# Kernel optimization log

Hardware: AMD Instinct MI355X
Metric: run time of the kernel (lower is better)

## Reference

```python
import jax, jax.numpy as jnp
import numpy as np

LEVELS = 3

def _db4_filters():
    s3 = np.sqrt(3.0)
    h0 = np.array([(1 + s3), (3 + s3), (3 - s3), (1 - s3)], dtype=np.float32) / (4 * np.sqrt(2.0))
    h1 = np.array([(-1) ** k * h0[3 - k] for k in range(4)], dtype=np.float32)
    return jnp.asarray(h0), jnp.asarray(h1)


def _dwt_1d(x, h0, h1):
    """Single-level db4 DWT along last axis, periodization boundary.
    x: (..., L) with L even -> (lo, hi) each (..., L//2).
    Matches torch: circular pad (left=1, right=2), conv1d (cross-correlation), stride-2 downsample.
    """
    L = x.shape[-1]
    xp = jnp.concatenate([x[..., -1:], x, x[..., :2]], axis=-1)  # circular pad -> (..., L+3)
    # full conv output has length L; only 4 taps, fuse as shifted adds
    lo = h0[0] * xp[..., 0:L] + h0[1] * xp[..., 1:L + 1] + h0[2] * xp[..., 2:L + 2] + h0[3] * xp[..., 3:L + 3]
    hi = h1[0] * xp[..., 0:L] + h1[1] * xp[..., 1:L + 1] + h1[2] * xp[..., 2:L + 2] + h1[3] * xp[..., 3:L + 3]
    return lo[..., ::2], hi[..., ::2]


def _dwt_2d(x, h0, h1):
    """x: (B,C,H,W) -> LL,LH,HL,HH each (B,C,H//2,W//2). Separable: rows (W) then cols (H)."""
    Lr, Hr = _dwt_1d(x, h0, h1)                       # (B,C,H,W/2)
    Lr_t = jnp.swapaxes(Lr, -1, -2)                   # (B,C,W/2,H)
    Hr_t = jnp.swapaxes(Hr, -1, -2)
    LL, LH = _dwt_1d(Lr_t, h0, h1)                    # (B,C,W/2,H/2)
    HL, HH = _dwt_1d(Hr_t, h0, h1)
    LL = jnp.swapaxes(LL, -1, -2)                     # (B,C,H/2,W/2)
    LH = jnp.swapaxes(LH, -1, -2)
    HL = jnp.swapaxes(HL, -1, -2)
    HH = jnp.swapaxes(HH, -1, -2)
    return LL, LH, HL, HH


def _forward(x):
    h0, h1 = _db4_filters()
    details = []  # (LH, HL, HH) per level, level 0 = finest
    cur = x
    for _ in range(LEVELS):
        LL, LH, HL, HH = _dwt_2d(cur, h0, h1)
        details.append((LH, HL, HH))
        cur = LL
    # coeffs_to_im: tile LL top-left, then wrap detail subbands coarsest->finest
    out = cur
    for level in reversed(range(LEVELS)):
        LH, HL, HH = details[level]
        top = jnp.concatenate([out, LH], axis=-1)
        bot = jnp.concatenate([HL, HH], axis=-1)
        out = jnp.concatenate([top, bot], axis=-2)
    return out


def setup_inputs() -> dict:
    key = jax.random.key(0)
    x = jax.random.normal(key, (8, 16, 512, 512), dtype=jnp.float32)
    return {"x": x}


def reference(x):
    return _forward(x)
```

## Files before the change

### kernel.cpp

```cpp
#include <hip/hip_runtime.h>


constexpr int TI = 16;
constexpr int TJ = 32;
constexpr int ROWS = 2 * TI + 2;
constexpr int COLS = 2 * TJ + 2;
constexpr int LDS_STRIDE = COLS + 2;

__global__ __launch_bounds__(256)
void dwt_level(const float* __restrict__ src, int N,
               float* __restrict__ out,
               float* __restrict__ ll, int ll_rs, size_t ll_cs)
{
    const int S = N >> 1;
    const int mask = N - 1;
    __shared__ float tile[ROWS][LDS_STRIDE];

    const int tx = threadIdx.x;
    const int ty = threadIdx.y;
    const int tid = ty * 32 + tx;
    const int j0 = blockIdx.x * TJ;
    const int i0 = blockIdx.y * TI;
    const int ch = blockIdx.z;

    const float* s = src + (size_t)ch * N * N;
    const int gr0 = 2 * i0 - 1;
    const int gc0 = 2 * j0 - 1;

    for (int k = tid; k < ROWS * COLS; k += 256) {
        const int r = k / COLS;
        const int c = k - r * COLS;
        const int gr = (gr0 + r) & mask;
        const int gc = (gc0 + c) & mask;
        tile[r][c] = s[(size_t)gr * N + gc];
    }
    __syncthreads();

    const float h0[4] = { 0.4829629131445341f,  0.8365163037378079f,
                          0.2241438680420134f, -0.1294095225512604f };
    const float h1[4] = { -0.1294095225512604f, -0.2241438680420134f,
                           0.8365163037378079f, -0.4829629131445341f };

    float* outc = out + (size_t)ch * (512 * 512);
    float* llc  = ll  + (size_t)ch * ll_cs;

    #pragma unroll
    for (int rr = 0; rr < 2; ++rr) {
        const int i = ty + rr * 8;
        const int j = tx;
        float a_ll = 0.f, a_lh = 0.f, a_hl = 0.f, a_hh = 0.f;
        #pragma unroll
        for (int p = 0; p < 4; ++p) {
            const float v0 = tile[2 * i + p][2 * j + 0];
            const float v1 = tile[2 * i + p][2 * j + 1];
            const float v2 = tile[2 * i + p][2 * j + 2];
            const float v3 = tile[2 * i + p][2 * j + 3];
            const float lo = h0[0] * v0 + h0[1] * v1 + h0[2] * v2 + h0[3] * v3;
            const float hi = h1[0] * v0 + h1[1] * v1 + h1[2] * v2 + h1[3] * v3;
            a_ll += h0[p] * lo;
            a_lh += h1[p] * lo;
            a_hl += h0[p] * hi;
            a_hh += h1[p] * hi;
        }
        const int gi = i0 + i;
        const int gj = j0 + j;
        llc[(size_t)gi * ll_rs + gj]            = a_ll;
        outc[(size_t)gi * 512 + (S + gj)]       = a_lh;
        outc[(size_t)(S + gi) * 512 + gj]       = a_hl;
        outc[(size_t)(S + gi) * 512 + (S + gj)] = a_hh;
    }
}

extern "C" void kernel_launch(void* const* d_in, const int* in_sizes, int n_in,
                              void* d_out, int out_size, void* d_ws, size_t ws_size,
                              hipStream_t stream) {
    const float* x = (const float*)d_in[0];
    float* out = (float*)d_out;
    const int C = in_sizes[0] / (512 * 512);

    float* ll1 = (float*)d_ws;
    float* ll2 = ll1 + (size_t)C * 256 * 256;

    dim3 blk(32, 8);
    dwt_level<<<dim3(256 / TJ, 256 / TI, C), blk, 0, stream>>>(
        x, 512, out, ll1, 256, (size_t)256 * 256);
    dwt_level<<<dim3(128 / TJ, 128 / TI, C), blk, 0, stream>>>(
        ll1, 256, out, ll2, 128, (size_t)128 * 128);
    dwt_level<<<dim3(64 / TJ, 64 / TI, C), blk, 0, stream>>>(
        ll2, 128, out, out, 512, (size_t)512 * 512);
}
```

Before: 265.8 us.

## Fuse all three DWT levels into one kernel with LDS-resident intermediates

Replaces three per-level kernel launches with a single kernel. Each block loads a 64x128 input tile plus halo (using float4 loads) into LDS, computes the level-1 LL subband into a second LDS buffer, then level-2 LL into a third, and writes the detail subbands directly to the output. This removes the global-memory round trips for the intermediate LL images and two launch overheads. The cost is redundant halo recomputation, large LDS use per block that limits occupancy, and a small grid (4x8xC blocks).

```diff
diff --git a/kernel.cpp b/kernel.cpp
--- a/kernel.cpp
+++ b/kernel.cpp
@@ -1,39 +1,44 @@
 #include <hip/hip_runtime.h>
 
 
-constexpr int TI = 16;
-constexpr int TJ = 32;
-constexpr int ROWS = 2 * TI + 2;
-constexpr int COLS = 2 * TJ + 2;
-constexpr int LDS_STRIDE = COLS + 2;
+constexpr int IN_R = 78;
+constexpr int IN_CV = 36;
+constexpr int IN_C = IN_CV * 4;
+constexpr int L1_R = 38, L1_C = 70, L1_S = 72;
+constexpr int L2_R = 18, L2_C = 34, L2_S = 36;
 
 __global__ __launch_bounds__(256)
-void dwt_level(const float* __restrict__ src, int N,
-               float* __restrict__ out,
-               float* __restrict__ ll, int ll_rs, size_t ll_cs)
+void dwt_fused(const float* __restrict__ x, float* __restrict__ out)
 {
-    const int S = N >> 1;
-    const int mask = N - 1;
-    __shared__ float tile[ROWS][LDS_STRIDE];
+    __shared__ float IN[IN_R * IN_C];
+    __shared__ float L1[L1_R * L1_S];
+    __shared__ float L2[L2_R * L2_S];
 
-    const int tx = threadIdx.x;
-    const int ty = threadIdx.y;
-    const int tid = ty * 32 + tx;
-    const int j0 = blockIdx.x * TJ;
-    const int i0 = blockIdx.y * TI;
-    const int ch = blockIdx.z;
+    const int tid = threadIdx.x;
+    const int cb  = blockIdx.x;
+    const int b   = blockIdx.y;
+    const int ch  = blockIdx.z;
 
-    const float* s = src + (size_t)ch * N * N;
-    const int gr0 = 2 * i0 - 1;
-    const int gc0 = 2 * j0 - 1;
+    const float* s = x   + (size_t)ch * (512 * 512);
+    float*       o = out + (size_t)ch * (512 * 512);
 
-    for (int k = tid; k < ROWS * COLS; k += 256) {
-        const int r = k / COLS;
-        const int c = k - r * COLS;
-        const int gr = (gr0 + r) & mask;
-        const int gc = (gc0 + c) & mask;
-        tile[r][c] = s[(size_t)gr * N + gc];
+    const int r0 = 64 * b - 7;
+    const int c0 = 128 * cb - 8;
+
+    float4 v[11]; int lof[11];
+    #pragma unroll
+    for (int k = 0; k < 11; ++k) {
+        int idx = tid + 256 * k;
+        if (idx > IN_R * IN_CV - 1) idx = IN_R * IN_CV - 1;
+        const int r = idx / IN_CV, m = idx - r * IN_CV;
+        const int gr = (r0 + r) & 511;
+        const int gc = (c0 + 4 * m) & 511;
+        v[k] = *reinterpret_cast<const float4*>(s + (size_t)gr * 512 + gc);
+        lof[k] = r * IN_C + 4 * m;
     }
+    #pragma unroll
+    for (int k = 0; k < 11; ++k)
+        *reinterpret_cast<float4*>(&IN[lof[k]]) = v[k];
     __syncthreads();
 
     const float h0[4] = { 0.4829629131445341f,  0.8365163037378079f,
@@ -41,33 +46,90 @@
     const float h1[4] = { -0.1294095225512604f, -0.2241438680420134f,
                            0.8365163037378079f, -0.4829629131445341f };
 
-    float* outc = out + (size_t)ch * (512 * 512);
-    float* llc  = ll  + (size_t)ch * ll_cs;
+    #pragma unroll
+    for (int k = 0; k < 11; ++k) {
+        int idx = tid + 256 * k;
+        if (idx > L1_R * L1_C - 1) idx = L1_R * L1_C - 1;
+        const int r = idx / L1_C, m = idx - r * L1_C;
+        float a = 0.f;
+        #pragma unroll
+        for (int p = 0; p < 4; ++p) {
+            const float* row = &IN[(2 * r + p) * IN_C + 2 * m + 1];
+            a += h0[p] * (h0[0]*row[0] + h0[1]*row[1] + h0[2]*row[2] + h0[3]*row[3]);
+        }
+        L1[r * L1_S + m] = a;
+    }
 
     #pragma unroll
-    for (int rr = 0; rr < 2; ++rr) {
-        const int i = ty + rr * 8;
-        const int j = tx;
-        float a_ll = 0.f, a_lh = 0.f, a_hl = 0.f, a_hh = 0.f;
+    for (int k = 0; k < 8; ++k) {
+        const int idx = tid + 256 * k;
+        const int i = idx >> 6, j = idx & 63;
+        float lh = 0.f, hl = 0.f, hh = 0.f;
         #pragma unroll
         for (int p = 0; p < 4; ++p) {
-            const float v0 = tile[2 * i + p][2 * j + 0];
-            const float v1 = tile[2 * i + p][2 * j + 1];
-            const float v2 = tile[2 * i + p][2 * j + 2];
-            const float v3 = tile[2 * i + p][2 * j + 3];
-            const float lo = h0[0] * v0 + h0[1] * v1 + h0[2] * v2 + h0[3] * v3;
-            const float hi = h1[0] * v0 + h1[1] * v1 + h1[2] * v2 + h1[3] * v3;
-            a_ll += h0[p] * lo;
-            a_lh += h1[p] * lo;
-            a_hl += h0[p] * hi;
-            a_hh += h1[p] * hi;
+            const float* row = &IN[(2 * i + 6 + p) * IN_C + 2 * j + 7];
+            const float v0 = row[0], v1 = row[1], v2 = row[2], v3 = row[3];
+            const float lo = h0[0]*v0 + h0[1]*v1 + h0[2]*v2 + h0[3]*v3;
+            const float hi = h1[0]*v0 + h1[1]*v1 + h1[2]*v2 + h1[3]*v3;
+            lh += h1[p] * lo; hl += h0[p] * hi; hh += h1[p] * hi;
         }
-        const int gi = i0 + i;
-        const int gj = j0 + j;
-        llc[(size_t)gi * ll_rs + gj]            = a_ll;
-        outc[(size_t)gi * 512 + (S + gj)]       = a_lh;
-        outc[(size_t)(S + gi) * 512 + gj]       = a_hl;
-        outc[(size_t)(S + gi) * 512 + (S + gj)] = a_hh;
+        const int gi = 32 * b + i, gj = 64 * cb + j;
+        o[(size_t)gi * 512 + (256 + gj)]         = lh;
+        o[(size_t)(256 + gi) * 512 + gj]         = hl;
+        o[(size_t)(256 + gi) * 512 + (256 + gj)] = hh;
+    }
+    __syncthreads();
+
+    #pragma unroll
+    for (int k = 0; k < 3; ++k) {
+        int idx = tid + 256 * k;
+        if (idx > L2_R * L2_C - 1) idx = L2_R * L2_C - 1;
+        const int r = idx / L2_C, m = idx - r * L2_C;
+        float a = 0.f;
+        #pragma unroll
+        for (int p = 0; p < 4; ++p) {
+            const float* row = &L1[(2 * r + p) * L1_S + 2 * m];
+            a += h0[p] * (h0[0]*row[0] + h0[1]*row[1] + h0[2]*row[2] + h0[3]*row[3]);
+        }
+        L2[r * L2_S + m] = a;
+    }
+
+    #pragma unroll
+    for (int k = 0; k < 2; ++k) {
+        const int idx = tid + 256 * k;
+        const int i = idx >> 5, j = idx & 31;
+        float lh = 0.f, hl = 0.f, hh = 0.f;
+        #pragma unroll
+        for (int p = 0; p < 4; ++p) {
+            const float* row = &L1[(2 * i + 2 + p) * L1_S + 2 * j + 2];
+            const float v0 = row[0], v1 = row[1], v2 = row[2], v3 = row[3];
+            const float lo = h0[0]*v0 + h0[1]*v1 + h0[2]*v2 + h0[3]*v3;
+            const float hi = h1[0]*v0 + h1[1]*v1 + h1[2]*v2 + h1[3]*v3;
+            lh += h1[p] * lo; hl += h0[p] * hi; hh += h1[p] * hi;
+        }
+        const int gi = 16 * b + i, gj = 32 * cb + j;
+        o[(size_t)gi * 512 + (128 + gj)]         = lh;
+        o[(size_t)(128 + gi) * 512 + gj]         = hl;
+        o[(size_t)(128 + gi) * 512 + (128 + gj)] = hh;
+    }
+    __syncthreads();
+
+    if (tid < 128) {
+        const int i = tid >> 4, j = tid & 15;
+        float ll = 0.f, lh = 0.f, hl = 0.f, hh = 0.f;
+        #pragma unroll
+        for (int p = 0; p < 4; ++p) {
+            const float* row = &L2[(2 * i + p) * L2_S + 2 * j];
+            const float v0 = row[0], v1 = row[1], v2 = row[2], v3 = row[3];
+            const float lo = h0[0]*v0 + h0[1]*v1 + h0[2]*v2 + h0[3]*v3;
+            const float hi = h1[0]*v0 + h1[1]*v1 + h1[2]*v2 + h1[3]*v3;
+            ll += h0[p] * lo; lh += h1[p] * lo; hl += h0[p] * hi; hh += h1[p] * hi;
+        }
+        const int gi = 8 * b + i, gj = 16 * cb + j;
+        o[(size_t)gi * 512 + gj]               = ll;
+        o[(size_t)gi * 512 + (64 + gj)]        = lh;
+        o[(size_t)(64 + gi) * 512 + gj]        = hl;
+        o[(size_t)(64 + gi) * 512 + (64 + gj)] = hh;
     }
 }
 
@@ -77,15 +139,5 @@
     const float* x = (const float*)d_in[0];
     float* out = (float*)d_out;
     const int C = in_sizes[0] / (512 * 512);
-
-    float* ll1 = (float*)d_ws;
-    float* ll2 = ll1 + (size_t)C * 256 * 256;
-
-    dim3 blk(32, 8);
-    dwt_level<<<dim3(256 / TJ, 256 / TI, C), blk, 0, stream>>>(
-        x, 512, out, ll1, 256, (size_t)256 * 256);
-    dwt_level<<<dim3(128 / TJ, 128 / TI, C), blk, 0, stream>>>(
-        ll1, 256, out, ll2, 128, (size_t)128 * 128);
-    dwt_level<<<dim3(64 / TJ, 64 / TI, C), blk, 0, stream>>>(
-        ll2, 128, out, out, 512, (size_t)512 * 512);
+    dwt_fused<<<dim3(4, 8, C), dim3(256), 0, stream>>>(x, out);
 }
```

Result: faster. 243.0 us (-8.6%).
